# Kernel tuning notes

Hardware: AMD Instinct MI355X
Metric: run time of the kernel (lower is better)

## Reference

```python
import jax, jax.numpy as jnp
import numpy as np

B, N, K, F, OUT = 32, 2000, 32, 64, 128

def setup_inputs() -> dict:
    key = jax.random.key(0)
    k1, k2, k3, k4, k5 = jax.random.split(key, 5)
    x = jax.random.normal(k1, (B, N, F), dtype=jnp.float32)
    neighborhood = jax.random.randint(k2, (N, K), 0, N, dtype=jnp.int64)
    distances = jax.random.uniform(k3, (N, K), dtype=jnp.float32)
    # Linear(k*(F+1), OUT): torch default init scale ~ 1/sqrt(fan_in)
    fan_in = K * (F + 1)
    W = jax.random.normal(k4, (OUT, fan_in), dtype=jnp.float32) / np.sqrt(fan_in)
    b = jax.random.normal(k5, (OUT,), dtype=jnp.float32) / np.sqrt(fan_in)
    return {"x": x, "neighborhood": neighborhood, "distances": distances, "W": W, "b": b}

def reference(x, neighborhood, distances, W, b):
    batch, seq_len, feat = x.shape          # [B, N, F]
    k = neighborhood.shape[1]
    gathered = x[:, neighborhood, :]        # [B, N, K, F] gather over sequence dim
    d = jnp.broadcast_to(distances[None, :, :, None], (batch, seq_len, k, 1))
    h = jnp.concatenate([gathered, d], axis=-1)        # [B, N, K, F+1]
    h = h.reshape(batch, seq_len, k * (feat + 1))      # [B, N, K*(F+1)]
    out = jnp.einsum('bnf,of->bno', h, W) + b          # [B, N, OUT]
    return out
```

## Files before the change

### kernel.cpp

```cpp
#include <hip/hip_runtime.h>
#include <hip/hip_bf16.h>
#include <stdint.h>

typedef __attribute__((ext_vector_type(8)))  __bf16   bf16x8;
typedef __attribute__((ext_vector_type(16))) float    f32x16;
typedef __attribute__((ext_vector_type(8)))  float    f32x8;

#define NB   32
#define NN   2000
#define NK   32
#define NF   64
#define NOUT 128
#define NSTEP 130

#define GLOBAL_AS __attribute__((address_space(1)))
#define LDS_AS    __attribute__((address_space(3)))
#define SB() __builtin_amdgcn_sched_barrier(0)

__global__ void kprep(const float* __restrict__ x, const float* __restrict__ dist,
                      const float* __restrict__ W,
                      __bf16* __restrict__ xb2, __bf16* __restrict__ db,
                      __bf16* __restrict__ Wf) {
  const int t = threadIdx.x;
  if (blockIdx.x < NN) {
    const int n = blockIdx.x;
    const int bb = t >> 3;
    const int f0 = (t & 7) << 3;
    const float* src = x + ((size_t)bb * NN + n) * NF + f0;
    f32x8 v = *(const f32x8*)src;
    bf16x8 r;
#pragma unroll
    for (int j = 0; j < 8; ++j) r[j] = (__bf16)v[j];
    const int off = ((f0 >> 4) << 10) + (((f0 >> 3) & 1) << 9) + (bb << 4);
    *(bf16x8*)((char*)xb2 + ((size_t)n << 12) + off) = r;
    if (t < NK) db[n * NK + t] = (__bf16)dist[n * NK + t];
  } else {
    const int kstep = blockIdx.x - NN;
    const int lane = t & 63;
    const int wv = t >> 6;
    const int o = wv * 32 + (lane & 31);
    const int kbase = kstep * 16 + (lane >> 5) * 8;
    bf16x8 r;
#pragma unroll
    for (int j = 0; j < 8; ++j) {
      const int kg = kbase + j;
      const int c = (kg < 2048) ? ((kg >> 6) * 65 + (kg & 63)) : ((kg - 2048) * 65 + 64);
      r[j] = (__bf16)W[(size_t)o * 2080 + c];
    }
    *(bf16x8*)(Wf + (((size_t)kstep * 256 + t) << 3)) = r;
  }
}

__global__ __launch_bounds__(256, 2) void kmain(
    const int* __restrict__ nbrs, const float* __restrict__ bias,
    const __bf16* __restrict__ xb2, const __bf16* __restrict__ Wf,
    const __bf16* __restrict__ db, float* __restrict__ out) {
  __shared__ __align__(16) char lds[4][4][4096];

  const int n0   = blockIdx.x * 4;
  const int t    = threadIdx.x;
  const int lane = t & 63;
  const int w    = t >> 6;
  const int col  = lane & 31;
  const int half = lane >> 5;

  f32x16 acc0 = {}, acc1 = {}, acc2 = {}, acc3 = {};

  int myidx = 0;
  if (lane < NK) myidx = nbrs[(n0 + w) * NK + lane];

  const __bf16* wfp = Wf + (((size_t)(w * 64 + lane)) << 3);

  auto stage = [&](int buf, int c) {
    const int nb = __builtin_amdgcn_readlane(myidx, c);
    const char* g = (const char*)xb2 + ((size_t)nb << 12) + lane * 16;
    char* l = &lds[buf][w][0];
#pragma unroll
    for (int q = 0; q < 4; ++q)
      __builtin_amdgcn_global_load_lds(
          (const GLOBAL_AS uint32_t*)(g + (q << 10)),
          (LDS_AS uint32_t*)(l + (q << 10)), 16, 0, 0);
  };

  auto loadB = [&](bf16x8* B, int i) {
#pragma unroll
    for (int s = 0; s < 4; ++s)
      B[s] = *(const bf16x8*)(wfp + ((size_t)(i * 4 + s) << 11));
  };

  auto compute = [&](int buf, const bf16x8* B) {
    __builtin_amdgcn_s_setprio(1);
#pragma unroll
    for (int s = 0; s < 4; ++s) {
      const char* lb = &lds[buf][0][0] + (s << 10) + lane * 16;
      bf16x8 a0 = *(const bf16x8*)(lb);
      bf16x8 a1 = *(const bf16x8*)(lb + 4096);
      bf16x8 a2 = *(const bf16x8*)(lb + 8192);
      bf16x8 a3 = *(const bf16x8*)(lb + 12288);
      acc0 = __builtin_amdgcn_mfma_f32_32x32x16_bf16(a0, B[s], acc0, 0, 0, 0);
      acc1 = __builtin_amdgcn_mfma_f32_32x32x16_bf16(a1, B[s], acc1, 0, 0, 0);
      acc2 = __builtin_amdgcn_mfma_f32_32x32x16_bf16(a2, B[s], acc2, 0, 0, 0);
      acc3 = __builtin_amdgcn_mfma_f32_32x32x16_bf16(a3, B[s], acc3, 0, 0, 0);
    }
    __builtin_amdgcn_s_setprio(0);
  };

  bf16x8 B0[4], B1[4];

  stage(0, 0); SB();
  loadB(B0, 0); SB();
  stage(1, 1); SB();

  for (int j = 0; j < 30; j += 2) {
    loadB(B1, j + 1); SB();
    stage((j + 2) & 3, j + 2); SB();
    asm volatile("s_waitcnt vmcnt(12)" ::: "memory");
    __builtin_amdgcn_s_barrier(); SB();
    compute(j & 3, B0);
    loadB(B0, j + 2); SB();
    stage((j + 3) & 3, j + 3); SB();
    asm volatile("s_waitcnt vmcnt(12)" ::: "memory");
    __builtin_amdgcn_s_barrier(); SB();
    compute((j + 1) & 3, B1);
  }
  loadB(B1, 31); SB();
  asm volatile("s_waitcnt vmcnt(8)" ::: "memory");
  __builtin_amdgcn_s_barrier(); SB();
  compute(30 & 3, B0);
  asm volatile("s_waitcnt vmcnt(0)" ::: "memory");
  __builtin_amdgcn_s_barrier(); SB();
  compute(31 & 3, B1);

#pragma unroll
  for (int s = 0; s < 2; ++s) {
    bf16x8 bfr = *(const bf16x8*)(wfp + ((size_t)(128 + s) << 11));
    const char* dbase = (const char*)db + (size_t)n0 * 64 + s * 32 + half * 16;
    bf16x8 d0 = *(const bf16x8*)(dbase);
    bf16x8 d1 = *(const bf16x8*)(dbase + 64);
    bf16x8 d2 = *(const bf16x8*)(dbase + 128);
    bf16x8 d3 = *(const bf16x8*)(dbase + 192);
    acc0 = __builtin_amdgcn_mfma_f32_32x32x16_bf16(d0, bfr, acc0, 0, 0, 0);
    acc1 = __builtin_amdgcn_mfma_f32_32x32x16_bf16(d1, bfr, acc1, 0, 0, 0);
    acc2 = __builtin_amdgcn_mfma_f32_32x32x16_bf16(d2, bfr, acc2, 0, 0, 0);
    acc3 = __builtin_amdgcn_mfma_f32_32x32x16_bf16(d3, bfr, acc3, 0, 0, 0);
  }

  const int o = w * 32 + col;
  const float bv = bias[o];
#pragma unroll
  for (int r = 0; r < 16; ++r) {
    const int row = (r & 3) + 8 * (r >> 2) + 4 * half;
    float* op = out + ((size_t)row * NN + n0) * NOUT + o;
    op[0 * NOUT] = acc0[r] + bv;
    op[1 * NOUT] = acc1[r] + bv;
    op[2 * NOUT] = acc2[r] + bv;
    op[3 * NOUT] = acc3[r] + bv;
  }
}

extern "C" void kernel_launch(void* const* d_in, const int* in_sizes, int n_in,
                              void* d_out, int out_size, void* d_ws, size_t ws_size,
                              hipStream_t stream) {
  const float* x    = (const float*)d_in[0];
  const int*   nbrs = (const int*)d_in[1];
  const float* dist = (const float*)d_in[2];
  const float* W    = (const float*)d_in[3];
  const float* bias = (const float*)d_in[4];
  float* out = (float*)d_out;

  char* ws = (char*)d_ws;
  __bf16* xb2 = (__bf16*)(ws);
  __bf16* Wf  = (__bf16*)(ws + 8192000);
  __bf16* db  = (__bf16*)(ws + 8192000 + 532480);

  kprep<<<NN + NSTEP, 256, 0, stream>>>(x, dist, W, xb2, db, Wf);
  kmain<<<NN / 4, 256, 0, stream>>>(nbrs, bias, xb2, Wf, db, out);
}
```

Measured before the change: 54.20 us.

## Split main kernel work into 2 nodes x 2 output halves per block and coalesce prep writes

The main kernel now handles 2 nodes per block instead of 4, with each wave covering one node and 64 output columns (two accumulators). The grid doubles and launch bounds allow 4 blocks per CU. The gather staging is split across wave pairs, and the prefetch depth changes to three stages ahead with retuned waitcnt values. The prep kernel transposes through shared memory so its bf16 layout writes become contiguous. The cost is twice as many weight-fragment loads per unit of work, since each block reuses W across fewer nodes.

```diff
diff --git a/kernel.cpp b/kernel.cpp
--- a/kernel.cpp
+++ b/kernel.cpp
@@ -23,6 +23,7 @@
                       __bf16* __restrict__ Wf) {
   const int t = threadIdx.x;
   if (blockIdx.x < NN) {
+    __shared__ __bf16 sm[32 * 66];
     const int n = blockIdx.x;
     const int bb = t >> 3;
     const int f0 = (t & 7) << 3;
@@ -31,8 +32,11 @@
     bf16x8 r;
 #pragma unroll
     for (int j = 0; j < 8; ++j) r[j] = (__bf16)v[j];
-    const int off = ((f0 >> 4) << 10) + (((f0 >> 3) & 1) << 9) + (bb << 4);
-    *(bf16x8*)((char*)xb2 + ((size_t)n << 12) + off) = r;
+    *(bf16x8*)&sm[bb * 66 + f0] = r;
+    __syncthreads();
+    const int col = t & 31, half = (t >> 5) & 1, s = t >> 6;
+    bf16x8 o = *(const bf16x8*)&sm[col * 66 + s * 16 + half * 8];
+    *(bf16x8*)((char*)xb2 + ((size_t)n << 12) + t * 16) = o;
     if (t < NK) db[n * NK + t] = (__bf16)dist[n * NK + t];
   } else {
     const int kstep = blockIdx.x - NN;
@@ -51,32 +55,34 @@
   }
 }
 
-__global__ __launch_bounds__(256, 2) void kmain(
+__global__ __launch_bounds__(256, 4) void kmain(
     const int* __restrict__ nbrs, const float* __restrict__ bias,
     const __bf16* __restrict__ xb2, const __bf16* __restrict__ Wf,
     const __bf16* __restrict__ db, float* __restrict__ out) {
-  __shared__ __align__(16) char lds[4][4][4096];
+  __shared__ __align__(16) char lds[4][2][4096];
 
-  const int n0   = blockIdx.x * 4;
+  const int n0   = blockIdx.x * 2;
   const int t    = threadIdx.x;
   const int lane = t & 63;
   const int w    = t >> 6;
   const int col  = lane & 31;
   const int half = lane >> 5;
+  const int np   = w >> 1;
+  const int ogp  = w & 1;
 
-  f32x16 acc0 = {}, acc1 = {}, acc2 = {}, acc3 = {};
+  f32x16 acc0 = {}, acc1 = {};
 
   int myidx = 0;
-  if (lane < NK) myidx = nbrs[(n0 + w) * NK + lane];
+  if (lane < NK) myidx = nbrs[(n0 + np) * NK + lane];
 
-  const __bf16* wfp = Wf + (((size_t)(w * 64 + lane)) << 3);
+  const char* wfb = (const char*)Wf + (ogp << 11) + lane * 16;
 
   auto stage = [&](int buf, int c) {
     const int nb = __builtin_amdgcn_readlane(myidx, c);
-    const char* g = (const char*)xb2 + ((size_t)nb << 12) + lane * 16;
-    char* l = &lds[buf][w][0];
+    const char* g = (const char*)xb2 + ((size_t)nb << 12) + (ogp << 11) + lane * 16;
+    char* l = &lds[buf][np][0] + (ogp << 11);
 #pragma unroll
-    for (int q = 0; q < 4; ++q)
+    for (int q = 0; q < 2; ++q)
       __builtin_amdgcn_global_load_lds(
           (const GLOBAL_AS uint32_t*)(g + (q << 10)),
           (LDS_AS uint32_t*)(l + (q << 10)), 16, 0, 0);
@@ -84,77 +90,79 @@
 
   auto loadB = [&](bf16x8* B, int i) {
 #pragma unroll
-    for (int s = 0; s < 4; ++s)
-      B[s] = *(const bf16x8*)(wfp + ((size_t)(i * 4 + s) << 11));
+    for (int s = 0; s < 4; ++s) {
+      B[s * 2 + 0] = *(const bf16x8*)(wfb + ((size_t)(i * 4 + s) << 12));
+      B[s * 2 + 1] = *(const bf16x8*)(wfb + ((size_t)(i * 4 + s) << 12) + 1024);
+    }
   };
 
   auto compute = [&](int buf, const bf16x8* B) {
     __builtin_amdgcn_s_setprio(1);
 #pragma unroll
     for (int s = 0; s < 4; ++s) {
-      const char* lb = &lds[buf][0][0] + (s << 10) + lane * 16;
-      bf16x8 a0 = *(const bf16x8*)(lb);
-      bf16x8 a1 = *(const bf16x8*)(lb + 4096);
-      bf16x8 a2 = *(const bf16x8*)(lb + 8192);
-      bf16x8 a3 = *(const bf16x8*)(lb + 12288);
-      acc0 = __builtin_amdgcn_mfma_f32_32x32x16_bf16(a0, B[s], acc0, 0, 0, 0);
-      acc1 = __builtin_amdgcn_mfma_f32_32x32x16_bf16(a1, B[s], acc1, 0, 0, 0);
-      acc2 = __builtin_amdgcn_mfma_f32_32x32x16_bf16(a2, B[s], acc2, 0, 0, 0);
-      acc3 = __builtin_amdgcn_mfma_f32_32x32x16_bf16(a3, B[s], acc3, 0, 0, 0);
+      bf16x8 a = *(const bf16x8*)(&lds[buf][np][0] + (s << 10) + lane * 16);
+      acc0 = __builtin_amdgcn_mfma_f32_32x32x16_bf16(a, B[s * 2 + 0], acc0, 0, 0, 0);
+      acc1 = __builtin_amdgcn_mfma_f32_32x32x16_bf16(a, B[s * 2 + 1], acc1, 0, 0, 0);
     }
     __builtin_amdgcn_s_setprio(0);
   };
 
-  bf16x8 B0[4], B1[4];
+  bf16x8 BA[8], BB[8];
 
   stage(0, 0); SB();
-  loadB(B0, 0); SB();
   stage(1, 1); SB();
+  loadB(BA, 0); SB();
+  __builtin_amdgcn_s_barrier();
+  stage(2, 2); SB();
 
-  for (int j = 0; j < 30; j += 2) {
-    loadB(B1, j + 1); SB();
-    stage((j + 2) & 3, j + 2); SB();
-    asm volatile("s_waitcnt vmcnt(12)" ::: "memory");
+  for (int j = 0; j < 28; j += 2) {
+    loadB(BB, j + 1); SB();
+    asm volatile("s_waitcnt vmcnt(10)" ::: "memory");
     __builtin_amdgcn_s_barrier(); SB();
-    compute(j & 3, B0);
-    loadB(B0, j + 2); SB();
     stage((j + 3) & 3, j + 3); SB();
-    asm volatile("s_waitcnt vmcnt(12)" ::: "memory");
+    compute(j & 3, BA);
+
+    loadB(BA, j + 2); SB();
+    asm volatile("s_waitcnt vmcnt(10)" ::: "memory");
     __builtin_amdgcn_s_barrier(); SB();
-    compute((j + 1) & 3, B1);
+    stage((j + 4) & 3, j + 4); SB();
+    compute((j + 1) & 3, BB);
   }
-  loadB(B1, 31); SB();
+  loadB(BB, 29); SB();
+  asm volatile("s_waitcnt vmcnt(10)" ::: "memory");
+  __builtin_amdgcn_s_barrier(); SB();
+  stage(31 & 3, 31); SB();
+  compute(28 & 3, BA);
+  loadB(BA, 30); SB();
+  asm volatile("s_waitcnt vmcnt(10)" ::: "memory");
+  __builtin_amdgcn_s_barrier(); SB();
+  compute(29 & 3, BB);
+  loadB(BB, 31); SB();
   asm volatile("s_waitcnt vmcnt(8)" ::: "memory");
   __builtin_amdgcn_s_barrier(); SB();
-  compute(30 & 3, B0);
+  compute(30 & 3, BA);
   asm volatile("s_waitcnt vmcnt(0)" ::: "memory");
   __builtin_amdgcn_s_barrier(); SB();
-  compute(31 & 3, B1);
+  compute(31 & 3, BB);
 
 #pragma unroll
   for (int s = 0; s < 2; ++s) {
-    bf16x8 bfr = *(const bf16x8*)(wfp + ((size_t)(128 + s) << 11));
-    const char* dbase = (const char*)db + (size_t)n0 * 64 + s * 32 + half * 16;
-    bf16x8 d0 = *(const bf16x8*)(dbase);
-    bf16x8 d1 = *(const bf16x8*)(dbase + 64);
-    bf16x8 d2 = *(const bf16x8*)(dbase + 128);
-    bf16x8 d3 = *(const bf16x8*)(dbase + 192);
-    acc0 = __builtin_amdgcn_mfma_f32_32x32x16_bf16(d0, bfr, acc0, 0, 0, 0);
-    acc1 = __builtin_amdgcn_mfma_f32_32x32x16_bf16(d1, bfr, acc1, 0, 0, 0);
-    acc2 = __builtin_amdgcn_mfma_f32_32x32x16_bf16(d2, bfr, acc2, 0, 0, 0);
-    acc3 = __builtin_amdgcn_mfma_f32_32x32x16_bf16(d3, bfr, acc3, 0, 0, 0);
+    bf16x8 dv = *(const bf16x8*)((const char*)db + (size_t)(n0 + np) * 64 + s * 32 + half * 16);
+    bf16x8 b0 = *(const bf16x8*)(wfb + ((size_t)(128 + s) << 12));
+    bf16x8 b1 = *(const bf16x8*)(wfb + ((size_t)(128 + s) << 12) + 1024);
+    acc0 = __builtin_amdgcn_mfma_f32_32x32x16_bf16(dv, b0, acc0, 0, 0, 0);
+    acc1 = __builtin_amdgcn_mfma_f32_32x32x16_bf16(dv, b1, acc1, 0, 0, 0);
   }
 
-  const int o = w * 32 + col;
-  const float bv = bias[o];
+  const int o0 = ogp * 64 + col;
+  const int nn = n0 + np;
+  const float bv0 = bias[o0], bv1 = bias[o0 + 32];
 #pragma unroll
   for (int r = 0; r < 16; ++r) {
     const int row = (r & 3) + 8 * (r >> 2) + 4 * half;
-    float* op = out + ((size_t)row * NN + n0) * NOUT + o;
-    op[0 * NOUT] = acc0[r] + bv;
-    op[1 * NOUT] = acc1[r] + bv;
-    op[2 * NOUT] = acc2[r] + bv;
-    op[3 * NOUT] = acc3[r] + bv;
+    float* op = out + ((size_t)row * NN + nn) * NOUT + o0;
+    op[0]  = acc0[r] + bv0;
+    op[32] = acc1[r] + bv1;
   }
 }
 
@@ -174,5 +182,5 @@
   __bf16* db  = (__bf16*)(ws + 8192000 + 532480);
 
   kprep<<<NN + NSTEP, 256, 0, stream>>>(x, dist, W, xb2, db, Wf);
-  kmain<<<NN / 4, 256, 0, stream>>>(nbrs, bias, xb2, Wf, db, out);
+  kmain<<<NN / 2, 256, 0, stream>>>(nbrs, bias, xb2, Wf, db, out);
 }
```

Result: slower. 67.55 us (+24.6%).
